# Performance work log

Measured on AMD Instinct MI355X. Metric: run time of the kernel, lower is better.

## Reference

```python
import jax, jax.numpy as jnp
import numpy as np

H = 12
D_MODEL = 768
D_K = D_MODEL // H  # 64


def setup_inputs() -> dict:
    key = jax.random.key(0)
    ks = jax.random.split(key, 16)
    B, S, D = 4, 1024, D_MODEL
    scale = 1.0 / np.sqrt(D)
    inp = {
        "query": jax.random.normal(ks[0], (B, S, D), jnp.float32),
        "key": jax.random.normal(ks[1], (B, S, D), jnp.float32),
        "value": jax.random.normal(ks[2], (B, S, D), jnp.float32),
        "times": jax.random.normal(ks[3], (2, B, S, D), jnp.float32),
        # learned params (Linear weights stored torch-style [out, in])
        "Wq": jax.random.normal(ks[4], (D, D), jnp.float32) * scale,
        "bq": jnp.zeros((D,), jnp.float32),
        "Wk": jax.random.normal(ks[5], (D, D), jnp.float32) * scale,
        "bk": jnp.zeros((D,), jnp.float32),
        "Wv": jax.random.normal(ks[6], (D, D), jnp.float32) * scale,
        "bv": jnp.zeros((D,), jnp.float32),
        "Wt": jax.random.normal(ks[7], (D, D), jnp.float32) * scale,
        "bt": jnp.zeros((D,), jnp.float32),
        "Wo": jax.random.normal(ks[8], (D, D), jnp.float32) * scale,
        "bo": jnp.zeros((D,), jnp.float32),
    }
    return inp


def _split_heads(x, B, S):
    # [B,S,D] -> [B,H,S,D_K]
    return x.reshape(B, S, H, D_K).transpose(0, 2, 1, 3)


def reference(query, key, value, times, Wq, bq, Wk, bk, Wv, bv, Wt, bt, Wo, bo):
    B, S, D = query.shape
    inv_sqrt_dk = 1.0 / jnp.sqrt(jnp.asarray(D_K, query.dtype))
    # q/k/v projections are identical across time-loop iterations; hoist them.
    q = _split_heads(query @ Wq.T + bq, B, S)   # [B,H,S,dk]
    k = _split_heads(key @ Wk.T + bk, B, S)
    v = _split_heads(value @ Wv.T + bv, B, S)
    x = jnp.zeros_like(q)
    n_times = times.shape[0]
    for i in range(n_times):  # small fixed loop over time embeddings
        t = _split_heads(times[i] @ Wt.T + bt, B, S)
        # dual-score attention: query.time + query.key, each scaled by 1/sqrt(d_k)
        scores = (jnp.einsum('bhqd,bhkd->bhqk', q, t)
                  + jnp.einsum('bhqd,bhkd->bhqk', q, k)) * inv_sqrt_dk
        p = jax.nn.softmax(scores, axis=-1)
        x = x + jnp.einsum('bhqk,bhkd->bhqd', p, v)
    x = x.transpose(0, 2, 1, 3).reshape(B, S, H * D_K)
    return x @ Wo.T + bo
```

## Files before the change

kernel.cpp:

```cpp
#include <hip/hip_runtime.h>
#include <hip/hip_fp16.h>

typedef _Float16 v8h __attribute__((ext_vector_type(8)));
typedef _Float16 v4h __attribute__((ext_vector_type(4)));
typedef float v4f __attribute__((ext_vector_type(4)));

#define MFMA_F16 __builtin_amdgcn_mfma_f32_16x16x32_f16
#define MFMA16_F16 __builtin_amdgcn_mfma_f32_16x16x16f16

__device__ static inline void async_copy16(const void* g, void* l) {
  __builtin_amdgcn_global_load_lds(
      (const __attribute__((address_space(1))) void*)g,
      (__attribute__((address_space(3))) void*)l, 16, 0, 0);
}

struct CastArgs {
  const float* src[10];
  _Float16* dst[10];
  int n8[10];
  float scale[10];
};
__global__ void cast_all(CastArgs a) {
  const int z = blockIdx.y;
  const int i = blockIdx.x * 256 + threadIdx.x;
  if (i >= a.n8[z]) return;
  const float sc = a.scale[z];
  const float* s = a.src[z] + (size_t)i * 8;
  const float4 f0 = *(const float4*)s;
  const float4 f1 = *(const float4*)(s + 4);
  v8h o = {(_Float16)(f0.x * sc), (_Float16)(f0.y * sc),
           (_Float16)(f0.z * sc), (_Float16)(f0.w * sc),
           (_Float16)(f1.x * sc), (_Float16)(f1.y * sc),
           (_Float16)(f1.z * sc), (_Float16)(f1.w * sc)};
  *(v8h*)(a.dst[z] + (size_t)i * 8) = o;
}

struct GemmArgs {
  const _Float16* A1[4]; const _Float16* A2[4];
  const _Float16* W1[4]; const _Float16* W2[4];
  const float* b1[4];    const float* b2[4];
  void* out[4];
  float bscale[4];
  int K[4];
  int mode[4];
};

__global__ __launch_bounds__(256) void gemm_mt(GemmArgs g) {
  __shared__ _Float16 a_lds[128 * 64];
  __shared__ _Float16 w_lds[128 * 64];
  const int z = blockIdx.z;
  const int KK = g.K[z];
  const int tid = threadIdx.x;
  const int w = tid >> 6, lane = tid & 63, quad = lane >> 4, l16 = lane & 15;
  const int m0 = blockIdx.x * 128, n0 = blockIdx.y * 128;
  const int wm = (w >> 1) * 64, wn = (w & 1) * 64;

  size_t srcOff[4]; int ldsOff[4];
  #pragma unroll
  for (int i = 0; i < 4; ++i) {
    const int c = i * 256 + tid, row = c >> 3, slot = c & 7;
    srcOff[i] = (size_t)row * 768 + (size_t)((slot ^ (row & 7)) * 8);
    ldsOff[i] = (i * 256 + w * 64) * 8;
  }

  v4f acc[4][4] = {};

  for (int k0 = 0; k0 < KK; k0 += 64) {
    const _Float16* Asrc = (k0 < 768) ? g.A1[z] : g.A2[z];
    const _Float16* Wsrc = (k0 < 768) ? g.W1[z] : g.W2[z];
    const int kc = (k0 < 768) ? k0 : k0 - 768;
    __syncthreads();
    #pragma unroll
    for (int i = 0; i < 4; ++i) {
      async_copy16(Asrc + (size_t)m0 * 768 + kc + srcOff[i], &a_lds[ldsOff[i]]);
      async_copy16(Wsrc + (size_t)n0 * 768 + kc + srcOff[i], &w_lds[ldsOff[i]]);
    }
    __syncthreads();

    #pragma unroll
    for (int kh = 0; kh < 2; ++kh) {
      v8h af[4], bf[4];
      #pragma unroll
      for (int mt = 0; mt < 4; ++mt) {
        const int r = wm + mt * 16 + l16;
        af[mt] = *(const v8h*)&a_lds[r * 64 + (((kh * 4 + quad) ^ (r & 7)) * 8)];
      }
      #pragma unroll
      for (int nt = 0; nt < 4; ++nt) {
        const int r = wn + nt * 16 + l16;
        bf[nt] = *(const v8h*)&w_lds[r * 64 + (((kh * 4 + quad) ^ (r & 7)) * 8)];
      }
      #pragma unroll
      for (int mt = 0; mt < 4; ++mt)
        #pragma unroll
        for (int nt = 0; nt < 4; ++nt)
          acc[mt][nt] = MFMA_F16(af[mt], bf[nt], acc[mt][nt], 0, 0, 0);
    }
  }

  const int mode = g.mode[z];
  #pragma unroll
  for (int nt = 0; nt < 4; ++nt) {
    const int col = n0 + wn + nt * 16 + l16;
    float bv = g.b1[z][col] * g.bscale[z];
    if (g.b2[z]) bv += g.b2[z][col];
    if (mode == 1) {
      _Float16* outp = (_Float16*)g.out[z];
      const int h = col >> 6, dk = col & 63;
      #pragma unroll
      for (int mt = 0; mt < 4; ++mt) {
        const int row = m0 + wm + mt * 16 + quad * 4;
        const int b = row >> 10, s = row & 1023;
        v4h pack = {(_Float16)(acc[mt][nt][0] + bv), (_Float16)(acc[mt][nt][1] + bv),
                    (_Float16)(acc[mt][nt][2] + bv), (_Float16)(acc[mt][nt][3] + bv)};
        *(v4h*)&outp[(size_t)((b * 12 + h) * 64 + dk) * 1024 + s] = pack;
      }
    } else {
      #pragma unroll
      for (int mt = 0; mt < 4; ++mt)
        #pragma unroll
        for (int r = 0; r < 4; ++r) {
          const int row = m0 + wm + mt * 16 + quad * 4 + r;
          const float v = acc[mt][nt][r] + bv;
          if (mode == 2) ((float*)g.out[z])[(size_t)row * 768 + col] = v;
          else ((_Float16*)g.out[z])[(size_t)row * 768 + col] = (_Float16)v;
        }
    }
  }
}

__global__ __launch_bounds__(256) void attn(
    const _Float16* __restrict__ Q,
    const _Float16* __restrict__ KT0, const _Float16* __restrict__ KT1,
    const _Float16* __restrict__ Vt,
    _Float16* __restrict__ X)
{
  __shared__ _Float16 kt0[2][2048];
  __shared__ _Float16 kt1[2][2048];
  __shared__ _Float16 vt[2][2048];

  const int tid = threadIdx.x;
  const int w = tid >> 6, lane = tid & 63, quad = lane >> 4, l16 = lane & 15;
  const int bh = blockIdx.y, b = bh / 12, h = bh % 12;
  const int q0 = blockIdx.x * 64;
  const size_t base = (size_t)b * 1024 * 768 + h * 64;

  const _Float16* KT0b = KT0 + base;
  const _Float16* KT1b = KT1 + base;
  const _Float16* Vtb = Vt + (size_t)bh * 64 * 1024;

  const int c = w * 64 + lane;
  const int ktRow = c >> 3, ktSlot = c & 7;
  const size_t ktOff = (size_t)ktRow * 768 + (size_t)((ktSlot ^ (ktRow & 7)) * 8);
  const int vRow = c >> 2, vSlot = c & 3;
  const size_t vOff = (size_t)vRow * 1024 + (size_t)((vSlot ^ (vRow & 3)) * 8);
  const int ldsOff = c * 8;

  auto stage = [&](int kv0, int buf) {
    async_copy16(KT0b + (size_t)kv0 * 768 + ktOff, &kt0[buf][ldsOff]);
    async_copy16(KT1b + (size_t)kv0 * 768 + ktOff, &kt1[buf][ldsOff]);
    async_copy16(Vtb + (size_t)kv0 + vOff, &vt[buf][ldsOff]);
  };

  const _Float16* Qw = Q + base + (size_t)(q0 + w * 16) * 768;
  const v8h qf0 = *(const v8h*)(Qw + (size_t)l16 * 768 + quad * 8);
  const v8h qf1 = *(const v8h*)(Qw + (size_t)l16 * 768 + 32 + quad * 8);

  v4f o[2][4] = {};
  float lsum[2] = {0.f, 0.f};

  stage(0, 0);
  for (int cc = 0; cc < 32; ++cc) {
    __syncthreads();
    if (cc < 31) stage((cc + 1) * 32, (cc + 1) & 1);
    const _Float16* k0p = &kt0[cc & 1][0];
    const _Float16* k1p = &kt1[cc & 1][0];
    const _Float16* vp = &vt[cc & 1][0];

    v4f s[2][2] = {};
    #pragma unroll
    for (int kvt = 0; kvt < 2; ++kvt) {
      const int r = kvt * 16 + l16, rw = r & 7;
      const v8h k00 = *(const v8h*)&k0p[r * 64 + ((quad ^ rw) * 8)];
      const v8h k01 = *(const v8h*)&k0p[r * 64 + (((4 + quad) ^ rw) * 8)];
      const v8h k10 = *(const v8h*)&k1p[r * 64 + ((quad ^ rw) * 8)];
      const v8h k11 = *(const v8h*)&k1p[r * 64 + (((4 + quad) ^ rw) * 8)];
      s[0][kvt] = MFMA_F16(k00, qf0, s[0][kvt], 0, 0, 0);
      s[0][kvt] = MFMA_F16(k01, qf1, s[0][kvt], 0, 0, 0);
      s[1][kvt] = MFMA_F16(k10, qf0, s[1][kvt], 0, 0, 0);
      s[1][kvt] = MFMA_F16(k11, qf1, s[1][kvt], 0, 0, 0);
    }

    v4h pb[2][2];
    #pragma unroll
    for (int t = 0; t < 2; ++t)
      #pragma unroll
      for (int kvt = 0; kvt < 2; ++kvt) {
        const float e0 = __expf(s[t][kvt][0]);
        const float e1 = __expf(s[t][kvt][1]);
        const float e2 = __expf(s[t][kvt][2]);
        const float e3 = __expf(s[t][kvt][3]);
        lsum[t] += (e0 + e1) + (e2 + e3);
        pb[t][kvt] = v4h{(_Float16)e0, (_Float16)e1, (_Float16)e2, (_Float16)e3};
      }

    #pragma unroll
    for (int dkt = 0; dkt < 4; ++dkt) {
      const int row = dkt * 16 + l16;
      #pragma unroll
      for (int kvt = 0; kvt < 2; ++kvt) {
        const int slot = (kvt * 2 + (quad >> 1)) ^ (row & 3);
        const v4h vf = *(const v4h*)&vp[row * 32 + slot * 8 + (quad & 1) * 4];
        o[0][dkt] = MFMA16_F16(vf, pb[0][kvt], o[0][dkt], 0, 0, 0);
        o[1][dkt] = MFMA16_F16(vf, pb[1][kvt], o[1][dkt], 0, 0, 0);
      }
    }
  }

  float s0 = lsum[0], s1 = lsum[1];
  s0 += __shfl_xor(s0, 16); s0 += __shfl_xor(s0, 32);
  s1 += __shfl_xor(s1, 16); s1 += __shfl_xor(s1, 32);
  const float i0 = 1.0f / s0, i1 = 1.0f / s1;

  _Float16* Xw = X + base + (size_t)(q0 + w * 16 + l16) * 768;
  #pragma unroll
  for (int dkt = 0; dkt < 4; ++dkt) {
    v4h pack;
    #pragma unroll
    for (int r = 0; r < 4; ++r)
      pack[r] = (_Float16)(o[0][dkt][r] * i0 + o[1][dkt][r] * i1);
    *(v4h*)&Xw[dkt * 16 + quad * 4] = pack;
  }
}

extern "C" void kernel_launch(void* const* d_in, const int* in_sizes, int n_in,
                              void* d_out, int out_size, void* d_ws, size_t ws_size,
                              hipStream_t stream) {
  const float* query = (const float*)d_in[0];
  const float* key   = (const float*)d_in[1];
  const float* value = (const float*)d_in[2];
  const float* times = (const float*)d_in[3];
  const float* Wq = (const float*)d_in[4];  const float* bq = (const float*)d_in[5];
  const float* Wk = (const float*)d_in[6];  const float* bk = (const float*)d_in[7];
  const float* Wv = (const float*)d_in[8];  const float* bv = (const float*)d_in[9];
  const float* Wt = (const float*)d_in[10]; const float* bt = (const float*)d_in[11];
  const float* Wo = (const float*)d_in[12]; const float* bo = (const float*)d_in[13];
  float* out = (float*)d_out;

  const size_t NELEM = (size_t)4096 * 768;
  const size_t WELEM = (size_t)768 * 768;

  char* ws = (char*)d_ws;
  size_t off = 0;
  auto alloc = [&](size_t bytes) {
    void* p = ws + off; off += (bytes + 255) & ~(size_t)255; return p;
  };
  _Float16* qh  = (_Float16*)alloc(NELEM * 2);
  _Float16* kh  = (_Float16*)alloc(NELEM * 2);
  _Float16* vh  = (_Float16*)alloc(NELEM * 2);
  _Float16* wqh = (_Float16*)alloc(WELEM * 2);
  _Float16* wkh = (_Float16*)alloc(WELEM * 2);
  _Float16* wvh = (_Float16*)alloc(WELEM * 2);
  _Float16* wth = (_Float16*)alloc(WELEM * 2);
  _Float16* woh = (_Float16*)alloc(WELEM * 2);
  _Float16* Qh  = (_Float16*)alloc(NELEM * 2);
  _Float16* KT0 = (_Float16*)alloc(NELEM * 2);
  _Float16* KT1 = (_Float16*)alloc(NELEM * 2);
  _Float16* Vt  = (_Float16*)alloc(NELEM * 2);
  _Float16* t0h = (_Float16*)d_out;
  _Float16* t1h = t0h + NELEM;
  _Float16* Xh = qh;

  CastArgs ca = {};
  const int nA8 = (int)(NELEM / 8), nW8 = (int)(WELEM / 8);
  const float* csrc[10] = {query, key, value, times, times + NELEM, Wq, Wk, Wv, Wt, Wo};
  _Float16* cdst[10] = {qh, kh, vh, t0h, t1h, wqh, wkh, wvh, wth, woh};
  for (int i = 0; i < 10; ++i) {
    ca.src[i] = csrc[i]; ca.dst[i] = cdst[i];
    ca.n8[i] = (i < 5) ? nA8 : nW8;
    ca.scale[i] = (i == 5) ? 0.125f : 1.0f;
  }
  cast_all<<<dim3((nA8 + 255) / 256, 10), 256, 0, stream>>>(ca);

  GemmArgs pa = {};
  pa.A1[0] = t0h; pa.A2[0] = kh; pa.W1[0] = wth; pa.W2[0] = wkh;
  pa.b1[0] = bt; pa.b2[0] = bk; pa.out[0] = KT0; pa.bscale[0] = 1.0f;
  pa.K[0] = 1536; pa.mode[0] = 0;
  pa.A1[1] = t1h; pa.A2[1] = kh; pa.W1[1] = wth; pa.W2[1] = wkh;
  pa.b1[1] = bt; pa.b2[1] = bk; pa.out[1] = KT1; pa.bscale[1] = 1.0f;
  pa.K[1] = 1536; pa.mode[1] = 0;
  pa.A1[2] = qh; pa.A2[2] = qh; pa.W1[2] = wqh; pa.W2[2] = wqh;
  pa.b1[2] = bq; pa.b2[2] = nullptr; pa.out[2] = Qh; pa.bscale[2] = 0.125f;
  pa.K[2] = 768; pa.mode[2] = 0;
  pa.A1[3] = vh; pa.A2[3] = vh; pa.W1[3] = wvh; pa.W2[3] = wvh;
  pa.b1[3] = bv; pa.b2[3] = nullptr; pa.out[3] = Vt; pa.bscale[3] = 1.0f;
  pa.K[3] = 768; pa.mode[3] = 1;
  gemm_mt<<<dim3(32, 6, 4), 256, 0, stream>>>(pa);

  attn<<<dim3(16, 48), 256, 0, stream>>>(Qh, KT0, KT1, Vt, Xh);

  GemmArgs oa = {};
  oa.A1[0] = Xh; oa.A2[0] = Xh; oa.W1[0] = woh; oa.W2[0] = woh;
  oa.b1[0] = bo; oa.b2[0] = nullptr; oa.out[0] = out; oa.bscale[0] = 1.0f;
  oa.K[0] = 768; oa.mode[0] = 2;
  gemm_mt<<<dim3(32, 6, 1), 256, 0, stream>>>(oa);
}
```

Measured before the change: 240.8 us.

## Double attention KV chunk to 64, fold log2e into Q, MFMA row sums

The attention loop now processes 64 keys per stage instead of 32, halving the number of barriers and pipeline iterations. log2(e) is folded into the Q scale so the kernel can use raw exp2 instead of __expf. Softmax denominators are accumulated with an MFMA against a ones vector, which removes the scalar adds and the cross-lane shuffles. The V transpose layout is permuted at write time so each lane reads one 16-byte v8h and splits it for two MFMAs. The trade-off is double the LDS footprint and more registers, which may lower occupancy.

```diff
diff --git a/kernel.cpp b/kernel.cpp
--- a/kernel.cpp
+++ b/kernel.cpp
@@ -7,6 +7,7 @@
 
 #define MFMA_F16 __builtin_amdgcn_mfma_f32_16x16x32_f16
 #define MFMA16_F16 __builtin_amdgcn_mfma_f32_16x16x16f16
+#define EXP2F __builtin_amdgcn_exp2f
 
 __device__ static inline void async_copy16(const void* g, void* l) {
   __builtin_amdgcn_global_load_lds(
@@ -111,9 +112,10 @@
       for (int mt = 0; mt < 4; ++mt) {
         const int row = m0 + wm + mt * 16 + quad * 4;
         const int b = row >> 10, s = row & 1023;
+        const int sp = (s & ~31) | ((s & 12) << 1) | ((s & 16) >> 2);
         v4h pack = {(_Float16)(acc[mt][nt][0] + bv), (_Float16)(acc[mt][nt][1] + bv),
                     (_Float16)(acc[mt][nt][2] + bv), (_Float16)(acc[mt][nt][3] + bv)};
-        *(v4h*)&outp[(size_t)((b * 12 + h) * 64 + dk) * 1024 + s] = pack;
+        *(v4h*)&outp[(size_t)((b * 12 + h) * 64 + dk) * 1024 + sp] = pack;
       }
     } else {
       #pragma unroll
@@ -135,9 +137,9 @@
     const _Float16* __restrict__ Vt,
     _Float16* __restrict__ X)
 {
-  __shared__ _Float16 kt0[2][2048];
-  __shared__ _Float16 kt1[2][2048];
-  __shared__ _Float16 vt[2][2048];
+  __shared__ _Float16 kt0[2][64 * 64];
+  __shared__ _Float16 kt1[2][64 * 64];
+  __shared__ _Float16 vt[2][64 * 64];
 
   const int tid = threadIdx.x;
   const int w = tid >> 6, lane = tid & 63, quad = lane >> 4, l16 = lane & 15;
@@ -149,78 +151,85 @@
   const _Float16* KT1b = KT1 + base;
   const _Float16* Vtb = Vt + (size_t)bh * 64 * 1024;
 
-  const int c = w * 64 + lane;
-  const int ktRow = c >> 3, ktSlot = c & 7;
-  const size_t ktOff = (size_t)ktRow * 768 + (size_t)((ktSlot ^ (ktRow & 7)) * 8);
-  const int vRow = c >> 2, vSlot = c & 3;
-  const size_t vOff = (size_t)vRow * 1024 + (size_t)((vSlot ^ (vRow & 3)) * 8);
-  const int ldsOff = c * 8;
-
+  size_t ktOff[2], vOff[2]; int ldsOff[2];
+  #pragma unroll
+  for (int i = 0; i < 2; ++i) {
+    const int c = i * 256 + w * 64 + lane, row = c >> 3, slot = c & 7;
+    const int logical = slot ^ (row & 7);
+    ktOff[i] = (size_t)row * 768 + (size_t)(logical * 8);
+    vOff[i] = (size_t)row * 1024 + (size_t)(logical * 8);
+    ldsOff[i] = c * 8;
+  }
   auto stage = [&](int kv0, int buf) {
-    async_copy16(KT0b + (size_t)kv0 * 768 + ktOff, &kt0[buf][ldsOff]);
-    async_copy16(KT1b + (size_t)kv0 * 768 + ktOff, &kt1[buf][ldsOff]);
-    async_copy16(Vtb + (size_t)kv0 + vOff, &vt[buf][ldsOff]);
+    #pragma unroll
+    for (int i = 0; i < 2; ++i) {
+      async_copy16(KT0b + (size_t)kv0 * 768 + ktOff[i], &kt0[buf][ldsOff[i]]);
+      async_copy16(KT1b + (size_t)kv0 * 768 + ktOff[i], &kt1[buf][ldsOff[i]]);
+      async_copy16(Vtb + (size_t)kv0 + vOff[i], &vt[buf][ldsOff[i]]);
+    }
   };
 
   const _Float16* Qw = Q + base + (size_t)(q0 + w * 16) * 768;
   const v8h qf0 = *(const v8h*)(Qw + (size_t)l16 * 768 + quad * 8);
   const v8h qf1 = *(const v8h*)(Qw + (size_t)l16 * 768 + 32 + quad * 8);
 
+  const v4h ones = {(_Float16)1.f, (_Float16)1.f, (_Float16)1.f, (_Float16)1.f};
   v4f o[2][4] = {};
-  float lsum[2] = {0.f, 0.f};
+  v4f osum[2] = {};
 
   stage(0, 0);
-  for (int cc = 0; cc < 32; ++cc) {
+  for (int cc = 0; cc < 16; ++cc) {
     __syncthreads();
-    if (cc < 31) stage((cc + 1) * 32, (cc + 1) & 1);
+    if (cc < 15) stage((cc + 1) * 64, (cc + 1) & 1);
     const _Float16* k0p = &kt0[cc & 1][0];
     const _Float16* k1p = &kt1[cc & 1][0];
     const _Float16* vp = &vt[cc & 1][0];
 
-    v4f s[2][2] = {};
-    #pragma unroll
-    for (int kvt = 0; kvt < 2; ++kvt) {
+    v4f s[2][4];
+    #pragma unroll
+    for (int kvt = 0; kvt < 4; ++kvt) {
       const int r = kvt * 16 + l16, rw = r & 7;
       const v8h k00 = *(const v8h*)&k0p[r * 64 + ((quad ^ rw) * 8)];
       const v8h k01 = *(const v8h*)&k0p[r * 64 + (((4 + quad) ^ rw) * 8)];
       const v8h k10 = *(const v8h*)&k1p[r * 64 + ((quad ^ rw) * 8)];
       const v8h k11 = *(const v8h*)&k1p[r * 64 + (((4 + quad) ^ rw) * 8)];
-      s[0][kvt] = MFMA_F16(k00, qf0, s[0][kvt], 0, 0, 0);
+      s[0][kvt] = MFMA_F16(k00, qf0, v4f{}, 0, 0, 0);
       s[0][kvt] = MFMA_F16(k01, qf1, s[0][kvt], 0, 0, 0);
-      s[1][kvt] = MFMA_F16(k10, qf0, s[1][kvt], 0, 0, 0);
+      s[1][kvt] = MFMA_F16(k10, qf0, v4f{}, 0, 0, 0);
       s[1][kvt] = MFMA_F16(k11, qf1, s[1][kvt], 0, 0, 0);
     }
 
-    v4h pb[2][2];
+    v4h pb[2][4];
     #pragma unroll
     for (int t = 0; t < 2; ++t)
       #pragma unroll
-      for (int kvt = 0; kvt < 2; ++kvt) {
-        const float e0 = __expf(s[t][kvt][0]);
-        const float e1 = __expf(s[t][kvt][1]);
-        const float e2 = __expf(s[t][kvt][2]);
-        const float e3 = __expf(s[t][kvt][3]);
-        lsum[t] += (e0 + e1) + (e2 + e3);
-        pb[t][kvt] = v4h{(_Float16)e0, (_Float16)e1, (_Float16)e2, (_Float16)e3};
+      for (int kvt = 0; kvt < 4; ++kvt) {
+        pb[t][kvt] = v4h{(_Float16)EXP2F(s[t][kvt][0]),
+                         (_Float16)EXP2F(s[t][kvt][1]),
+                         (_Float16)EXP2F(s[t][kvt][2]),
+                         (_Float16)EXP2F(s[t][kvt][3])};
+        osum[t] = MFMA16_F16(ones, pb[t][kvt], osum[t], 0, 0, 0);
       }
 
     #pragma unroll
     for (int dkt = 0; dkt < 4; ++dkt) {
-      const int row = dkt * 16 + l16;
-      #pragma unroll
-      for (int kvt = 0; kvt < 2; ++kvt) {
-        const int slot = (kvt * 2 + (quad >> 1)) ^ (row & 3);
-        const v4h vf = *(const v4h*)&vp[row * 32 + slot * 8 + (quad & 1) * 4];
-        o[0][dkt] = MFMA16_F16(vf, pb[0][kvt], o[0][dkt], 0, 0, 0);
-        o[1][dkt] = MFMA16_F16(vf, pb[1][kvt], o[1][dkt], 0, 0, 0);
-      }
-    }
-  }
-
-  float s0 = lsum[0], s1 = lsum[1];
-  s0 += __shfl_xor(s0, 16); s0 += __shfl_xor(s0, 32);
-  s1 += __shfl_xor(s1, 16); s1 += __shfl_xor(s1, 32);
-  const float i0 = 1.0f / s0, i1 = 1.0f / s1;
+      const int row = dkt * 16 + l16, rw = row & 7;
+      #pragma unroll
+      for (int gph = 0; gph < 2; ++gph) {
+        const int phys = (gph * 4 + quad) ^ rw;
+        const v8h vv = *(const v8h*)&vp[row * 64 + phys * 8];
+        const v4h lo = {vv[0], vv[1], vv[2], vv[3]};
+        const v4h hi = {vv[4], vv[5], vv[6], vv[7]};
+        #pragma unroll
+        for (int t = 0; t < 2; ++t) {
+          o[t][dkt] = MFMA16_F16(lo, pb[t][gph * 2], o[t][dkt], 0, 0, 0);
+          o[t][dkt] = MFMA16_F16(hi, pb[t][gph * 2 + 1], o[t][dkt], 0, 0, 0);
+        }
+      }
+    }
+  }
+
+  const float i0 = 1.0f / osum[0][0], i1 = 1.0f / osum[1][0];
 
   _Float16* Xw = X + base + (size_t)(q0 + w * 16 + l16) * 768;
   #pragma unroll
@@ -249,6 +258,7 @@
 
   const size_t NELEM = (size_t)4096 * 768;
   const size_t WELEM = (size_t)768 * 768;
+  const float QSCALE = 0.125f * 1.4426950408889634f;
 
   char* ws = (char*)d_ws;
   size_t off = 0;
@@ -278,7 +288,7 @@
   for (int i = 0; i < 10; ++i) {
     ca.src[i] = csrc[i]; ca.dst[i] = cdst[i];
     ca.n8[i] = (i < 5) ? nA8 : nW8;
-    ca.scale[i] = (i == 5) ? 0.125f : 1.0f;
+    ca.scale[i] = (i == 5) ? QSCALE : 1.0f;
   }
   cast_all<<<dim3((nA8 + 255) / 256, 10), 256, 0, stream>>>(ca);
 
@@ -290,7 +300,7 @@
   pa.b1[1] = bt; pa.b2[1] = bk; pa.out[1] = KT1; pa.bscale[1] = 1.0f;
   pa.K[1] = 1536; pa.mode[1] = 0;
   pa.A1[2] = qh; pa.A2[2] = qh; pa.W1[2] = wqh; pa.W2[2] = wqh;
-  pa.b1[2] = bq; pa.b2[2] = nullptr; pa.out[2] = Qh; pa.bscale[2] = 0.125f;
+  pa.b1[2] = bq; pa.b2[2] = nullptr; pa.out[2] = Qh; pa.bscale[2] = QSCALE;
   pa.K[2] = 768; pa.mode[2] = 0;
   pa.A1[3] = vh; pa.A2[3] = vh; pa.W1[3] = wvh; pa.W2[3] = wvh;
   pa.b1[3] = bv; pa.b2[3] = nullptr; pa.out[3] = Vt; pa.bscale[3] = 1.0f;
```

Measured after the change: 237.8 us. About the same (-1.3%).
